# Performance work log

Measured on AMD Instinct MI355X. Metric: run time of the kernel, lower is better.

Reference implementation:

```python
import jax, jax.numpy as jnp
import numpy as np

EXTENT = 0.5       # init kwarg 'extent'
RES = 256          # init kwarg 'resolution'
BATCH = 8
N_PTS = 65536      # one 256x256 Fourier slice per image


def setup_inputs() -> dict:
    key = jax.random.key(0)
    k1, k2 = jax.random.split(key)
    # coordinates in [-extent, extent]
    x = (jax.random.uniform(k1, (BATCH, N_PTS, 3), dtype=jnp.float32) * 2.0 - 1.0) * EXTENT
    # learned volume parameter, matches 1e-5 * randn init
    volume = 1e-5 * jax.random.normal(k2, (RES, RES, RES), dtype=jnp.float32)
    return {"x": x, "volume": volume}


def _grid_sample_3d(vol, coords):
    """Trilinear grid sample, align_corners=False, padding_mode='zeros'.
    vol: [D, H, W]; coords: [..., 3] with (x, y, z) in [-1, 1] indexing (W, H, D).
    Matches torch.nn.functional.grid_sample(mode='bilinear') for 5D input.
    """
    D, H, W = vol.shape
    gx, gy, gz = coords[..., 0], coords[..., 1], coords[..., 2]
    # unnormalize (align_corners=False): ix = ((x + 1) * W - 1) / 2
    ix = ((gx + 1.0) * W - 1.0) * 0.5
    iy = ((gy + 1.0) * H - 1.0) * 0.5
    iz = ((gz + 1.0) * D - 1.0) * 0.5
    x0 = jnp.floor(ix)
    y0 = jnp.floor(iy)
    z0 = jnp.floor(iz)
    tx = ix - x0  # fractional weights
    ty = iy - y0
    tz = iz - z0
    x0i = x0.astype(jnp.int32)
    y0i = y0.astype(jnp.int32)
    z0i = z0.astype(jnp.int32)

    def corner(dz, dy, dx):
        xi = x0i + dx
        yi = y0i + dy
        zi = z0i + dz
        valid = (xi >= 0) & (xi < W) & (yi >= 0) & (yi < H) & (zi >= 0) & (zi < D)
        v = vol[jnp.clip(zi, 0, D - 1), jnp.clip(yi, 0, H - 1), jnp.clip(xi, 0, W - 1)]
        return jnp.where(valid, v, jnp.zeros((), vol.dtype))

    wx0, wy0, wz0 = 1.0 - tx, 1.0 - ty, 1.0 - tz
    out = (corner(0, 0, 0) * wz0 * wy0 * wx0
           + corner(0, 0, 1) * wz0 * wy0 * tx
           + corner(0, 1, 0) * wz0 * ty * wx0
           + corner(0, 1, 1) * wz0 * ty * tx
           + corner(1, 0, 0) * tz * wy0 * wx0
           + corner(1, 0, 1) * tz * wy0 * tx
           + corner(1, 1, 0) * tz * ty * wx0
           + corner(1, 1, 1) * tz * ty * tx)
    return out


def reference(x, volume):
    # original: grid_sample(100 * volume.repeat(B,...), x/(2*extent)*2)
    #    the linear interpolation (mathematically identical).
    coords = x / EXTENT  # [B, n_pts, 3] in [-1, 1]
    return 100.0 * _grid_sample_3d(volume, coords)  # [B, n_pts]
```

## Files before the change

### kernel.cpp

```cpp
#include <hip/hip_runtime.h>


#define RES 256
#define TZ 4
#define TY 8
#define NZT 64
#define NYT 32
#define NBKT 2048
#define CAP 318
#define NROW 45
#define LDSF (NROW * 256)

typedef float vfloat4 __attribute__((ext_vector_type(4)));


__device__ __forceinline__ void setup_c(
    float rx, float ry, float rz,
    int& r00, int& r01, int& r10, int& r11, int& xc0, int& xc1,
    float& wx0, float& wx1, float& wy0, float& wy1, float& wz0, float& wz1)
{
    float ix = ((rx * 2.0f + 1.0f) * (float)RES - 1.0f) * 0.5f;
    float iy = ((ry * 2.0f + 1.0f) * (float)RES - 1.0f) * 0.5f;
    float iz = ((rz * 2.0f + 1.0f) * (float)RES - 1.0f) * 0.5f;

    float x0f = floorf(ix), y0f = floorf(iy), z0f = floorf(iz);
    float tx = ix - x0f, ty = iy - y0f, tz = iz - z0f;

    int x0 = (int)x0f, y0 = (int)y0f, z0 = (int)z0f;
    int x1 = x0 + 1, y1 = y0 + 1, z1 = z0 + 1;

    wx0 = (x0 >= 0 && x0 < RES) ? (1.0f - tx) : 0.0f;
    wx1 = (x1 >= 0 && x1 < RES) ? tx : 0.0f;
    wy0 = (y0 >= 0 && y0 < RES) ? (1.0f - ty) : 0.0f;
    wy1 = (y1 >= 0 && y1 < RES) ? ty : 0.0f;
    wz0 = (z0 >= 0 && z0 < RES) ? (1.0f - tz) : 0.0f;
    wz1 = (z1 >= 0 && z1 < RES) ? tz : 0.0f;

    xc0 = min(max(x0, 0), RES - 1); xc1 = min(max(x1, 0), RES - 1);
    int yc0 = min(max(y0, 0), RES - 1), yc1 = min(max(y1, 0), RES - 1);
    int zc0 = min(max(z0, 0), RES - 1), zc1 = min(max(z1, 0), RES - 1);

    r00 = (zc0 * RES + yc0) * RES;
    r01 = (zc0 * RES + yc1) * RES;
    r10 = (zc1 * RES + yc0) * RES;
    r11 = (zc1 * RES + yc1) * RES;
}

__device__ __forceinline__ float trilerp_g(
    const float* __restrict__ vol,
    int r00, int r01, int r10, int r11, int xc0, int xc1,
    float wx0, float wx1, float wy0, float wy1, float wz0, float wz1)
{
    float v000 = vol[r00 + xc0];
    float v001 = vol[r00 + xc1];
    float v010 = vol[r01 + xc0];
    float v011 = vol[r01 + xc1];
    float v100 = vol[r10 + xc0];
    float v101 = vol[r10 + xc1];
    float v110 = vol[r11 + xc0];
    float v111 = vol[r11 + xc1];
    float c00 = v000 * wx0 + v001 * wx1;
    float c01 = v010 * wx0 + v011 * wx1;
    float c10 = v100 * wx0 + v101 * wx1;
    float c11 = v110 * wx0 + v111 * wx1;
    float c0 = c00 * wy0 + c01 * wy1;
    float c1 = c10 * wy0 + c11 * wy1;
    return 100.0f * (c0 * wz0 + c1 * wz1);
}

__device__ __forceinline__ float interp_point(
    const float* __restrict__ vol, float rx, float ry, float rz)
{
    int r00, r01, r10, r11, x0, x1;
    float wx0, wx1, wy0, wy1, wz0, wz1;
    setup_c(rx, ry, rz, r00, r01, r10, r11, x0, x1,
            wx0, wx1, wy0, wy1, wz0, wz1);
    return trilerp_g(vol, r00, r01, r10, r11, x0, x1,
                     wx0, wx1, wy0, wy1, wz0, wz1);
}


__global__ __launch_bounds__(256) void VolumeExplicit_scatter_kernel(
    const float* __restrict__ x,
    const float* __restrict__ vol,
    float* __restrict__ out,
    vfloat4* __restrict__ sorted,
    unsigned* __restrict__ cursor)
{
    __shared__ unsigned lh[NBKT];
    __shared__ unsigned lbase[NBKT];
    int t = threadIdx.x;
    int base_i = blockIdx.x * 1024;

    for (int b = t; b < NBKT; b += 256) lh[b] = 0;
    __syncthreads();

    float px[4], py[4], pz[4];
    int bk[4];
    unsigned lr[4];
    #pragma unroll
    for (int k = 0; k < 4; ++k) {
        int i = base_i + (k << 8) + t;
        px[k] = __builtin_nontemporal_load(&x[3 * i + 0]);
        py[k] = __builtin_nontemporal_load(&x[3 * i + 1]);
        pz[k] = __builtin_nontemporal_load(&x[3 * i + 2]);
        float iy = ((py[k] * 2.0f + 1.0f) * (float)RES - 1.0f) * 0.5f;
        float iz = ((pz[k] * 2.0f + 1.0f) * (float)RES - 1.0f) * 0.5f;
        int y0 = (int)floorf(iy);
        int z0 = (int)floorf(iz);
        int yc0 = min(max(y0, 0), RES - 1);
        int zc0 = min(max(z0, 0), RES - 1);
        int b_ = (zc0 >> 2) * NYT + (yc0 >> 3);
        bk[k] = b_;
        lr[k] = atomicAdd(&lh[b_], 1u);
    }
    __syncthreads();

    for (int b = t; b < NBKT; b += 256) {
        unsigned c = lh[b];
        lbase[b] = c ? atomicAdd(&cursor[b], c) : 0u;
    }
    __syncthreads();

    #pragma unroll
    for (int k = 0; k < 4; ++k) {
        int i = base_i + (k << 8) + t;
        unsigned pos = lbase[bk[k]] + lr[k];
        if (pos < CAP) {
            vfloat4 v;
            v.x = px[k]; v.y = py[k]; v.z = pz[k];
            v.w = __uint_as_float((unsigned)i);
            sorted[bk[k] * CAP + pos] = v;
        } else {
            out[i] = interp_point(vol, px[k], py[k], pz[k]);
        }
    }
}


__global__ __launch_bounds__(256) void VolumeExplicit_gather_kernel(
    const vfloat4* __restrict__ sorted,
    const unsigned* __restrict__ cursor,
    const float* __restrict__ vol,
    float* __restrict__ out)
{
    __shared__ float smem[LDSF];

    int t = threadIdx.x;
    int B = blockIdx.x;
    int xcd = B & 7;
    int j = (B >> 3) & 7;
    int yt = B >> 6;
    int zt = xcd * 8 + j;
    int bucket = zt * NYT + yt;

    for (int k = t; k < NROW * 64; k += 256) {
        int q = k >> 6;
        int lane = k & 63;
        int zr = q / 9;
        int yr = q - zr * 9;
        int gz = min(zt * TZ + zr, RES - 1);
        int gy = min(yt * TY + yr, RES - 1);
        const vfloat4* src =
            reinterpret_cast<const vfloat4*>(vol + ((gz << 8) + gy) * 256);
        reinterpret_cast<vfloat4*>(smem)[(q << 6) + lane] = src[lane];
    }
    __syncthreads();

    unsigned count = cursor[bucket];
    if (count > CAP) count = CAP;

    for (int s = t; s < (int)count; s += 256) {
        vfloat4 p = __builtin_nontemporal_load(&sorted[bucket * CAP + s]);

        float ix = ((p.x * 2.0f + 1.0f) * (float)RES - 1.0f) * 0.5f;
        float iy = ((p.y * 2.0f + 1.0f) * (float)RES - 1.0f) * 0.5f;
        float iz = ((p.z * 2.0f + 1.0f) * (float)RES - 1.0f) * 0.5f;

        float x0f = floorf(ix), y0f = floorf(iy), z0f = floorf(iz);
        float tx = ix - x0f, ty = iy - y0f, tz = iz - z0f;

        int x0 = (int)x0f, y0 = (int)y0f, z0 = (int)z0f;
        int x1 = x0 + 1, y1 = y0 + 1, z1 = z0 + 1;

        float wx0 = (x0 >= 0 && x0 < RES) ? (1.0f - tx) : 0.0f;
        float wx1 = (x1 >= 0 && x1 < RES) ? tx : 0.0f;
        float wy0 = (y0 >= 0 && y0 < RES) ? (1.0f - ty) : 0.0f;
        float wy1 = (y1 >= 0 && y1 < RES) ? ty : 0.0f;
        float wz0 = (z0 >= 0 && z0 < RES) ? (1.0f - tz) : 0.0f;
        float wz1 = (z1 >= 0 && z1 < RES) ? tz : 0.0f;

        int xc0 = min(max(x0, 0), RES - 1), xc1 = min(max(x1, 0), RES - 1);
        int yc0 = min(max(y0, 0), RES - 1), yc1 = min(max(y1, 0), RES - 1);
        int zc0 = min(max(z0, 0), RES - 1), zc1 = min(max(z1, 0), RES - 1);

        int zl0 = zc0 - zt * TZ, zl1 = zc1 - zt * TZ;
        int yl0 = yc0 - yt * TY, yl1 = yc1 - yt * TY;

        int r00 = ((zl0 * 9 + yl0) << 8);
        int r01 = ((zl0 * 9 + yl1) << 8);
        int r10 = ((zl1 * 9 + yl0) << 8);
        int r11 = ((zl1 * 9 + yl1) << 8);

        float v000 = smem[r00 + xc0];
        float v001 = smem[r00 + xc1];
        float v010 = smem[r01 + xc0];
        float v011 = smem[r01 + xc1];
        float v100 = smem[r10 + xc0];
        float v101 = smem[r10 + xc1];
        float v110 = smem[r11 + xc0];
        float v111 = smem[r11 + xc1];

        float c00 = v000 * wx0 + v001 * wx1;
        float c01 = v010 * wx0 + v011 * wx1;
        float c10 = v100 * wx0 + v101 * wx1;
        float c11 = v110 * wx0 + v111 * wx1;
        float c0 = c00 * wy0 + c01 * wy1;
        float c1 = c10 * wy0 + c11 * wy1;
        float o = 100.0f * (c0 * wz0 + c1 * wz1);

        __builtin_nontemporal_store(o, &out[__float_as_uint(p.w)]);
    }
}


__global__ __launch_bounds__(256) void VolumeExplicit_29257317220866_kernel(
    const float* __restrict__ x,
    const float* __restrict__ vol,
    float* __restrict__ out,
    int n)
{
    int tid = blockIdx.x * blockDim.x + threadIdx.x;
    int half = n >> 1;
    if (tid >= half) return;
    int iA = tid;
    int iB = tid + half;

    float oA, oB;
    {
        float rx = __builtin_nontemporal_load(&x[3 * iA + 0]);
        float ry = __builtin_nontemporal_load(&x[3 * iA + 1]);
        float rz = __builtin_nontemporal_load(&x[3 * iA + 2]);
        oA = interp_point(vol, rx, ry, rz);
    }
    {
        float rx = __builtin_nontemporal_load(&x[3 * iB + 0]);
        float ry = __builtin_nontemporal_load(&x[3 * iB + 1]);
        float rz = __builtin_nontemporal_load(&x[3 * iB + 2]);
        oB = interp_point(vol, rx, ry, rz);
    }

    __builtin_nontemporal_store(oA, &out[iA]);
    __builtin_nontemporal_store(oB, &out[iB]);
}

extern "C" void kernel_launch(void* const* d_in, const int* in_sizes, int n_in,
                              void* d_out, int out_size, void* d_ws, size_t ws_size,
                              hipStream_t stream) {
    const float* x   = (const float*)d_in[0];
    const float* vol = (const float*)d_in[1];
    float* out = (float*)d_out;

    int n = out_size;
    size_t need = 8192 + (size_t)NBKT * CAP * sizeof(vfloat4);

    if (n == 524288 && d_ws != nullptr && ws_size >= need) {
        unsigned* cursor = (unsigned*)d_ws;
        vfloat4* sorted  = (vfloat4*)((char*)d_ws + 8192);

        hipMemsetAsync(cursor, 0, NBKT * sizeof(unsigned), stream);
        VolumeExplicit_scatter_kernel<<<n / 1024, 256, 0, stream>>>(
            x, vol, out, sorted, cursor);
        VolumeExplicit_gather_kernel<<<NBKT, 256, 0, stream>>>(
            sorted, cursor, vol, out);
    } else {
        int half = n >> 1;
        int block = 256;
        int grid = (half + block - 1) / block;
        VolumeExplicit_29257317220866_kernel<<<grid, block, 0, stream>>>(x, vol, out, n);
    }
}
```

Measured before the change: 138.2 us.

## Double-buffer volume tiles in gather kernel with async global-to-LDS loads

The gather kernel now launches 256 persistent blocks instead of 2048, and each block walks 8 consecutive y-tiles of one z-slab. The next tile is staged into a second LDS buffer with global_load_lds while the current bucket's points are interpolated, so volume loading overlaps compute. Bucket capacity is raised so fewer points overflow to the slow direct-gather fallback, and the helper functions are inlined. The trade-off is less parallelism (256 blocks with 90KB LDS each) and a full vmcnt wait plus barrier per tile. Neighbouring y-tiles also share halo rows that are still loaded twice.

Result: faster. 133.7 us (-3.2%).

```diff
diff --git a/kernel.cpp b/kernel.cpp
--- a/kernel.cpp
+++ b/kernel.cpp
@@ -7,17 +7,16 @@
 #define NZT 64
 #define NYT 32
 #define NBKT 2048
-#define CAP 318
+#define CAP 352
 #define NROW 45
-#define LDSF (NROW * 256)
+#define TILEF (NROW * 256)
+#define NTHREADS 256
 
 typedef float vfloat4 __attribute__((ext_vector_type(4)));
 
 
-__device__ __forceinline__ void setup_c(
-    float rx, float ry, float rz,
-    int& r00, int& r01, int& r10, int& r11, int& xc0, int& xc1,
-    float& wx0, float& wx1, float& wy0, float& wy1, float& wz0, float& wz1)
+__device__ __forceinline__ float interp_point(
+    const float* __restrict__ vol, float rx, float ry, float rz)
 {
     float ix = ((rx * 2.0f + 1.0f) * (float)RES - 1.0f) * 0.5f;
     float iy = ((ry * 2.0f + 1.0f) * (float)RES - 1.0f) * 0.5f;
@@ -29,28 +28,22 @@
     int x0 = (int)x0f, y0 = (int)y0f, z0 = (int)z0f;
     int x1 = x0 + 1, y1 = y0 + 1, z1 = z0 + 1;
 
-    wx0 = (x0 >= 0 && x0 < RES) ? (1.0f - tx) : 0.0f;
-    wx1 = (x1 >= 0 && x1 < RES) ? tx : 0.0f;
-    wy0 = (y0 >= 0 && y0 < RES) ? (1.0f - ty) : 0.0f;
-    wy1 = (y1 >= 0 && y1 < RES) ? ty : 0.0f;
-    wz0 = (z0 >= 0 && z0 < RES) ? (1.0f - tz) : 0.0f;
-    wz1 = (z1 >= 0 && z1 < RES) ? tz : 0.0f;
-
-    xc0 = min(max(x0, 0), RES - 1); xc1 = min(max(x1, 0), RES - 1);
+    float wx0 = (x0 >= 0 && x0 < RES) ? (1.0f - tx) : 0.0f;
+    float wx1 = (x1 >= 0 && x1 < RES) ? tx : 0.0f;
+    float wy0 = (y0 >= 0 && y0 < RES) ? (1.0f - ty) : 0.0f;
+    float wy1 = (y1 >= 0 && y1 < RES) ? ty : 0.0f;
+    float wz0 = (z0 >= 0 && z0 < RES) ? (1.0f - tz) : 0.0f;
+    float wz1 = (z1 >= 0 && z1 < RES) ? tz : 0.0f;
+
+    int xc0 = min(max(x0, 0), RES - 1), xc1 = min(max(x1, 0), RES - 1);
     int yc0 = min(max(y0, 0), RES - 1), yc1 = min(max(y1, 0), RES - 1);
     int zc0 = min(max(z0, 0), RES - 1), zc1 = min(max(z1, 0), RES - 1);
 
-    r00 = (zc0 * RES + yc0) * RES;
-    r01 = (zc0 * RES + yc1) * RES;
-    r10 = (zc1 * RES + yc0) * RES;
-    r11 = (zc1 * RES + yc1) * RES;
-}
-
-__device__ __forceinline__ float trilerp_g(
-    const float* __restrict__ vol,
-    int r00, int r01, int r10, int r11, int xc0, int xc1,
-    float wx0, float wx1, float wy0, float wy1, float wz0, float wz1)
-{
+    int r00 = (zc0 * RES + yc0) * RES;
+    int r01 = (zc0 * RES + yc1) * RES;
+    int r10 = (zc1 * RES + yc0) * RES;
+    int r11 = (zc1 * RES + yc1) * RES;
+
     float v000 = vol[r00 + xc0];
     float v001 = vol[r00 + xc1];
     float v010 = vol[r01 + xc0];
@@ -59,6 +52,7 @@
     float v101 = vol[r10 + xc1];
     float v110 = vol[r11 + xc0];
     float v111 = vol[r11 + xc1];
+
     float c00 = v000 * wx0 + v001 * wx1;
     float c01 = v010 * wx0 + v011 * wx1;
     float c10 = v100 * wx0 + v101 * wx1;
@@ -66,17 +60,6 @@
     float c0 = c00 * wy0 + c01 * wy1;
     float c1 = c10 * wy0 + c11 * wy1;
     return 100.0f * (c0 * wz0 + c1 * wz1);
-}
-
-__device__ __forceinline__ float interp_point(
-    const float* __restrict__ vol, float rx, float ry, float rz)
-{
-    int r00, r01, r10, r11, x0, x1;
-    float wx0, wx1, wy0, wy1, wz0, wz1;
-    setup_c(rx, ry, rz, r00, r01, r10, r11, x0, x1,
-            wx0, wx1, wy0, wy1, wz0, wz1);
-    return trilerp_g(vol, r00, r01, r10, r11, x0, x1,
-                     wx0, wx1, wy0, wy1, wz0, wz1);
 }
 
 
@@ -130,10 +113,31 @@
             vfloat4 v;
             v.x = px[k]; v.y = py[k]; v.z = pz[k];
             v.w = __uint_as_float((unsigned)i);
-            sorted[bk[k] * CAP + pos] = v;
+            sorted[(size_t)bk[k] * CAP + pos] = v;
         } else {
             out[i] = interp_point(vol, px[k], py[k], pz[k]);
         }
+    }
+}
+
+
+__device__ __forceinline__ void stage_tile(
+    const float* __restrict__ vol, float* dst, int zt, int yt, int lane, int w)
+{
+    for (int q = w; q < NROW; q += 4) {
+        int zr = q / 9;
+        int yr = q - zr * 9;
+        int gz = min(zt * TZ + zr, RES - 1);
+        int gy = min(yt * TY + yr, RES - 1);
+        const float* src = vol + (size_t)(((gz << 8) + gy) << 8) + (lane << 2);
+#if __has_builtin(__builtin_amdgcn_global_load_lds)
+        __builtin_amdgcn_global_load_lds(
+            (const __attribute__((address_space(1))) void*)src,
+            (__attribute__((address_space(3))) void*)(dst + q * 256),
+            16, 0, 0);
+#else
+        *(vfloat4*)(dst + q * 256 + (lane << 2)) = *(const vfloat4*)src;
+#endif
     }
 }
 
@@ -144,82 +148,87 @@
     const float* __restrict__ vol,
     float* __restrict__ out)
 {
-    __shared__ float smem[LDSF];
+    extern __shared__ float smem[];
 
     int t = threadIdx.x;
+    int lane = t & 63;
+    int w = t >> 6;
     int B = blockIdx.x;
     int xcd = B & 7;
-    int j = (B >> 3) & 7;
-    int yt = B >> 6;
-    int zt = xcd * 8 + j;
-    int bucket = zt * NYT + yt;
-
-    for (int k = t; k < NROW * 64; k += 256) {
-        int q = k >> 6;
-        int lane = k & 63;
-        int zr = q / 9;
-        int yr = q - zr * 9;
-        int gz = min(zt * TZ + zr, RES - 1);
-        int gy = min(yt * TY + yr, RES - 1);
-        const vfloat4* src =
-            reinterpret_cast<const vfloat4*>(vol + ((gz << 8) + gy) * 256);
-        reinterpret_cast<vfloat4*>(smem)[(q << 6) + lane] = src[lane];
-    }
-    __syncthreads();
-
-    unsigned count = cursor[bucket];
-    if (count > CAP) count = CAP;
-
-    for (int s = t; s < (int)count; s += 256) {
-        vfloat4 p = __builtin_nontemporal_load(&sorted[bucket * CAP + s]);
-
-        float ix = ((p.x * 2.0f + 1.0f) * (float)RES - 1.0f) * 0.5f;
-        float iy = ((p.y * 2.0f + 1.0f) * (float)RES - 1.0f) * 0.5f;
-        float iz = ((p.z * 2.0f + 1.0f) * (float)RES - 1.0f) * 0.5f;
-
-        float x0f = floorf(ix), y0f = floorf(iy), z0f = floorf(iz);
-        float tx = ix - x0f, ty = iy - y0f, tz = iz - z0f;
-
-        int x0 = (int)x0f, y0 = (int)y0f, z0 = (int)z0f;
-        int x1 = x0 + 1, y1 = y0 + 1, z1 = z0 + 1;
-
-        float wx0 = (x0 >= 0 && x0 < RES) ? (1.0f - tx) : 0.0f;
-        float wx1 = (x1 >= 0 && x1 < RES) ? tx : 0.0f;
-        float wy0 = (y0 >= 0 && y0 < RES) ? (1.0f - ty) : 0.0f;
-        float wy1 = (y1 >= 0 && y1 < RES) ? ty : 0.0f;
-        float wz0 = (z0 >= 0 && z0 < RES) ? (1.0f - tz) : 0.0f;
-        float wz1 = (z1 >= 0 && z1 < RES) ? tz : 0.0f;
-
-        int xc0 = min(max(x0, 0), RES - 1), xc1 = min(max(x1, 0), RES - 1);
-        int yc0 = min(max(y0, 0), RES - 1), yc1 = min(max(y1, 0), RES - 1);
-        int zc0 = min(max(z0, 0), RES - 1), zc1 = min(max(z1, 0), RES - 1);
-
-        int zl0 = zc0 - zt * TZ, zl1 = zc1 - zt * TZ;
-        int yl0 = yc0 - yt * TY, yl1 = yc1 - yt * TY;
-
-        int r00 = ((zl0 * 9 + yl0) << 8);
-        int r01 = ((zl0 * 9 + yl1) << 8);
-        int r10 = ((zl1 * 9 + yl0) << 8);
-        int r11 = ((zl1 * 9 + yl1) << 8);
-
-        float v000 = smem[r00 + xc0];
-        float v001 = smem[r00 + xc1];
-        float v010 = smem[r01 + xc0];
-        float v011 = smem[r01 + xc1];
-        float v100 = smem[r10 + xc0];
-        float v101 = smem[r10 + xc1];
-        float v110 = smem[r11 + xc0];
-        float v111 = smem[r11 + xc1];
-
-        float c00 = v000 * wx0 + v001 * wx1;
-        float c01 = v010 * wx0 + v011 * wx1;
-        float c10 = v100 * wx0 + v101 * wx1;
-        float c11 = v110 * wx0 + v111 * wx1;
-        float c0 = c00 * wy0 + c01 * wy1;
-        float c1 = c10 * wy0 + c11 * wy1;
-        float o = 100.0f * (c0 * wz0 + c1 * wz1);
-
-        __builtin_nontemporal_store(o, &out[__float_as_uint(p.w)]);
+    int c = B >> 3;
+    int zt = (xcd << 3) | (c & 7);
+    int ytBase = (c >> 3) << 3;
+
+    stage_tile(vol, smem, zt, ytBase, lane, w);
+    asm volatile("s_waitcnt vmcnt(0)");
+    __syncthreads();
+
+    #pragma unroll 1
+    for (int k = 0; k < 8; ++k) {
+        if (k < 7)
+            stage_tile(vol, smem + ((k + 1) & 1) * TILEF, zt, ytBase + k + 1,
+                       lane, w);
+
+        int yt = ytBase + k;
+        int bucket = zt * NYT + yt;
+        unsigned count = cursor[bucket];
+        if (count > CAP) count = CAP;
+        const float* tile = smem + (k & 1) * TILEF;
+
+        for (int s = t; s < (int)count; s += NTHREADS) {
+            vfloat4 p = __builtin_nontemporal_load(&sorted[(size_t)bucket * CAP + s]);
+
+            float ix = ((p.x * 2.0f + 1.0f) * (float)RES - 1.0f) * 0.5f;
+            float iy = ((p.y * 2.0f + 1.0f) * (float)RES - 1.0f) * 0.5f;
+            float iz = ((p.z * 2.0f + 1.0f) * (float)RES - 1.0f) * 0.5f;
+
+            float x0f = floorf(ix), y0f = floorf(iy), z0f = floorf(iz);
+            float tx = ix - x0f, ty = iy - y0f, tz = iz - z0f;
+
+            int x0 = (int)x0f, y0 = (int)y0f, z0 = (int)z0f;
+            int x1 = x0 + 1, y1 = y0 + 1, z1 = z0 + 1;
+
+            float wx0 = (x0 >= 0 && x0 < RES) ? (1.0f - tx) : 0.0f;
+            float wx1 = (x1 >= 0 && x1 < RES) ? tx : 0.0f;
+            float wy0 = (y0 >= 0 && y0 < RES) ? (1.0f - ty) : 0.0f;
+            float wy1 = (y1 >= 0 && y1 < RES) ? ty : 0.0f;
+            float wz0 = (z0 >= 0 && z0 < RES) ? (1.0f - tz) : 0.0f;
+            float wz1 = (z1 >= 0 && z1 < RES) ? tz : 0.0f;
+
+            int xc0 = min(max(x0, 0), RES - 1), xc1 = min(max(x1, 0), RES - 1);
+            int yc0 = min(max(y0, 0), RES - 1), yc1 = min(max(y1, 0), RES - 1);
+            int zc0 = min(max(z0, 0), RES - 1), zc1 = min(max(z1, 0), RES - 1);
+
+            int zl0 = zc0 - zt * TZ, zl1 = zc1 - zt * TZ;
+            int yl0 = yc0 - yt * TY, yl1 = yc1 - yt * TY;
+
+            int r00 = ((zl0 * 9 + yl0) << 8);
+            int r01 = ((zl0 * 9 + yl1) << 8);
+            int r10 = ((zl1 * 9 + yl0) << 8);
+            int r11 = ((zl1 * 9 + yl1) << 8);
+
+            float v000 = tile[r00 + xc0];
+            float v001 = tile[r00 + xc1];
+            float v010 = tile[r01 + xc0];
+            float v011 = tile[r01 + xc1];
+            float v100 = tile[r10 + xc0];
+            float v101 = tile[r10 + xc1];
+            float v110 = tile[r11 + xc0];
+            float v111 = tile[r11 + xc1];
+
+            float c00 = v000 * wx0 + v001 * wx1;
+            float c01 = v010 * wx0 + v011 * wx1;
+            float c10 = v100 * wx0 + v101 * wx1;
+            float c11 = v110 * wx0 + v111 * wx1;
+            float c0 = c00 * wy0 + c01 * wy1;
+            float c1 = c10 * wy0 + c11 * wy1;
+            float o = 100.0f * (c0 * wz0 + c1 * wz1);
+
+            __builtin_nontemporal_store(o, &out[__float_as_uint(p.w)]);
+        }
+
+        asm volatile("s_waitcnt vmcnt(0)");
+        __syncthreads();
     }
 }
 
@@ -271,8 +280,8 @@
         hipMemsetAsync(cursor, 0, NBKT * sizeof(unsigned), stream);
         VolumeExplicit_scatter_kernel<<<n / 1024, 256, 0, stream>>>(
             x, vol, out, sorted, cursor);
-        VolumeExplicit_gather_kernel<<<NBKT, 256, 0, stream>>>(
-            sorted, cursor, vol, out);
+        VolumeExplicit_gather_kernel<<<256, NTHREADS,
+            2 * TILEF * sizeof(float), stream>>>(sorted, cursor, vol, out);
     } else {
         int half = n >> 1;
         int block = 256;
```
